# Performance work log

Measured on AMD Instinct MI355X. Metric: run time of the kernel, lower is better.

## Reference

```python
import jax, jax.numpy as jnp
import numpy as np

HIDDEN = 1024
HEADS = 16
HEAD_DIM = HIDDEN // HEADS


def rotate_half(x):
    x1, x2 = jnp.split(x, 2, axis=-1)
    return jnp.concatenate([-x2, x1], axis=-1)


def rope_cos_sin(T, head_dim):
    inv_freq = 1.0 / (10000.0 ** (jnp.arange(0, head_dim, 2, dtype=jnp.float32) / head_dim))
    pos = jnp.arange(T, dtype=jnp.float32)
    freqs = jnp.einsum('i,j->ij', pos, inv_freq)          # [T, head_dim/2]
    emb = jnp.concatenate([freqs, freqs], axis=-1)        # [T, head_dim]
    # broadcast shape [1, T, 1, head_dim]
    return jnp.cos(emb)[None, :, None, :], jnp.sin(emb)[None, :, None, :]


def setup_inputs() -> dict:
    key = jax.random.key(0)
    ks = jax.random.split(key, 9)
    B, T = 4, 2048
    s = 1.0 / np.sqrt(HIDDEN)
    x = jax.random.normal(ks[0], (B, T, HIDDEN), dtype=jnp.float32)
    Wq = jax.random.uniform(ks[1], (HIDDEN, HIDDEN), minval=-s, maxval=s, dtype=jnp.float32)
    bq = jax.random.uniform(ks[2], (HIDDEN,), minval=-s, maxval=s, dtype=jnp.float32)
    Wk = jax.random.uniform(ks[3], (HIDDEN, HIDDEN), minval=-s, maxval=s, dtype=jnp.float32)
    bk = jax.random.uniform(ks[4], (HIDDEN,), minval=-s, maxval=s, dtype=jnp.float32)
    Wv = jax.random.uniform(ks[5], (HIDDEN, HIDDEN), minval=-s, maxval=s, dtype=jnp.float32)
    bv = jax.random.uniform(ks[6], (HIDDEN,), minval=-s, maxval=s, dtype=jnp.float32)
    Wo = jax.random.uniform(ks[7], (HIDDEN, HIDDEN), minval=-s, maxval=s, dtype=jnp.float32)
    bo = jax.random.uniform(ks[8], (HIDDEN,), minval=-s, maxval=s, dtype=jnp.float32)
    return {"x": x, "Wq": Wq, "bq": bq, "Wk": Wk, "bk": bk,
            "Wv": Wv, "bv": bv, "Wo": Wo, "bo": bo}


def reference(x, Wq, bq, Wk, bk, Wv, bv, Wo, bo):
    B, T, _ = x.shape
    q = (x @ Wq + bq).reshape(B, T, HEADS, HEAD_DIM)
    k = (x @ Wk + bk).reshape(B, T, HEADS, HEAD_DIM)
    v = (x @ Wv + bv).reshape(B, T, HEADS, HEAD_DIM)
    cos, sin = rope_cos_sin(T, HEAD_DIM)
    q = q * cos + rotate_half(q) * sin
    k = k * cos + rotate_half(k) * sin
    scale = jnp.sqrt(jnp.float32(HEAD_DIM))
    scores = jnp.einsum('bqhd,bkhd->bhqk', q, k) / scale   # [B,H,T,T]
    causal = jnp.tril(jnp.ones((T, T), dtype=bool))
    scores = jnp.where(causal[None, None], scores, -jnp.inf)
    probs = jax.nn.softmax(scores, axis=-1)
    attn = jnp.einsum('bhqk,bkhd->bqhd', probs, v).reshape(B, T, HIDDEN)
    return attn @ Wo + bo
```

## Files before the change

### kernel.cpp

```cpp
#include <hip/hip_runtime.h>

typedef unsigned short u16;
typedef __attribute__((ext_vector_type(4))) float f32x4;
typedef __attribute__((ext_vector_type(16))) float f32x16;
typedef __attribute__((ext_vector_type(8))) short s16x8;

#define B_   4
#define T_   2048
#define H_   16
#define D_   64
#define HID  1024
#define BT   (B_*T_)
#define N3   3072

#define BARRIER() do { asm volatile("" ::: "memory"); __builtin_amdgcn_s_barrier(); asm volatile("" ::: "memory"); } while (0)

__device__ inline u16 f2b(float f) {
  union { float f; unsigned u; } v; v.f = f;
  unsigned u = v.u;
  unsigned r = (u + 0x7FFFu + ((u >> 16) & 1u)) >> 16;
  return (u16)r;
}

__device__ inline void gll16(const u16* g, u16* l) {
  __builtin_amdgcn_global_load_lds(
      (const __attribute__((address_space(1))) unsigned int*)g,
      (__attribute__((address_space(3))) unsigned int*)l, 16, 0, 0);
}

__device__ inline int swz8(int row) { return (row ^ (row >> 3)) & 7; }

__global__ void k_cast4(const float* __restrict__ src, u16* __restrict__ dst, int n4) {
  int i = blockIdx.x * blockDim.x + threadIdx.x;
  if (i >= n4) return;
  float4 v = ((const float4*)src)[i];
  ushort4 o;
  o.x = f2b(v.x); o.y = f2b(v.y); o.z = f2b(v.z); o.w = f2b(v.w);
  ((ushort4*)dst)[i] = o;
}

__global__ void k_ropetab(float2* __restrict__ tab) {
  int i = blockIdx.x * blockDim.x + threadIdx.x;
  int d = i & 31, t = i >> 5;
  float inv = expf(-0.28782313662425574f * (float)d);
  float ang = (float)t * inv;
  float c, s;
  sincosf(ang, &s, &c);
  tab[i] = make_float2(c, s);
}

__global__ __launch_bounds__(256) void k_packT(const float* __restrict__ W0,
                                               const float* __restrict__ W1,
                                               const float* __restrict__ W2,
                                               u16* __restrict__ Wt) {
  __shared__ float L[64][68];
  int n0 = blockIdx.x * 64, k0 = blockIdx.y * 64;
  int which = n0 >> 10;
  const float* W = (which == 0) ? W0 : (which == 1) ? W1 : W2;
  int nc = n0 & 1023;
  int tid = threadIdx.x;
  #pragma unroll
  for (int i = 0; i < 4; i++) {
    int ch = tid + 256 * i;
    int kr = ch >> 4, cc = ch & 15;
    float4 v = *(const float4*)(W + (size_t)(k0 + kr) * 1024 + nc + cc * 4);
    *(float4*)(&L[kr][cc * 4]) = v;
  }
  __syncthreads();
  #pragma unroll
  for (int i = 0; i < 2; i++) {
    int ch = tid + 256 * i;
    int nr = ch >> 3, ck = ch & 7;
    u16 tmp[8];
    #pragma unroll
    for (int j = 0; j < 8; j++) tmp[j] = f2b(L[ck * 8 + j][nr]);
    *(uint4*)(Wt + (size_t)(n0 + nr) * 1024 + k0 + ck * 8) = *(uint4*)tmp;
  }
}

__global__ __launch_bounds__(512, 2) void gemm256(
    const u16* __restrict__ A, const u16* __restrict__ Bt,
    const float* __restrict__ b0, const float* __restrict__ b1,
    const float* __restrict__ b2, const float2* __restrict__ tab,
    u16* __restrict__ outp)
{
  __shared__ __align__(16) char SM[135168];
  const int tid = threadIdx.x, lane = tid & 63, w = tid >> 6;
  const int l15 = lane & 15, g = lane >> 4;
  const int wm = (w >> 2) * 128, wn = (w & 3) * 64;
  const int mbase = blockIdx.y * 256, nbase = blockIdx.x * 256;
  const int K = 1024, NT = 16;
  f32x4 acc[8][4] = {};

  auto SHALF = [&](const u16* src, int base, int buf, int isB, int half, int t) {
    u16* dst = (u16*)(SM + buf * 65536 + isB * 32768 + half * 16384);
    #pragma unroll
    for (int i = 0; i < 2; i++) {
      int f = i * 512 + tid;
      int r = f >> 3, c = f & 7;
      int row = half * 128 + r;
      int cs = c ^ (row & 7);
      gll16(src + (size_t)(base + row) * K + t * 64 + cs * 8, dst + f * 8);
    }
  };
  auto RD = [&](const char* buf, int row, int kc) -> s16x8 {
    int slot = (kc * 4 + g) ^ (row & 7);
    return *(const s16x8*)(buf + row * 128 + slot * 16);
  };

  SHALF(A, mbase, 0, 0, 0, 0); SHALF(A, mbase, 0, 0, 1, 0);
  SHALF(Bt, nbase, 0, 1, 0, 0); SHALF(Bt, nbase, 0, 1, 1, 0);
  SHALF(Bt, nbase, 1, 1, 0, 1); SHALF(Bt, nbase, 1, 1, 1, 1);
  asm volatile("s_waitcnt vmcnt(4)" ::: "memory");
  BARRIER();

  s16x8 af[4][2], bf[4][2];
  for (int t = 0; t < NT; t++) {
    const char* Ab = SM + (t & 1) * 65536;
    const char* Bb = Ab + 32768;
    const int nxA = (t + 1) & 1;
    const int nxB = t & 1;

    #pragma unroll
    for (int mt = 0; mt < 4; mt++) {
      af[mt][0] = RD(Ab, wm + mt * 16 + l15, 0);
      af[mt][1] = RD(Ab, wm + mt * 16 + l15, 1);
    }
    #pragma unroll
    for (int nt = 0; nt < 2; nt++) {
      bf[nt][0] = RD(Bb, wn + nt * 16 + l15, 0);
      bf[nt][1] = RD(Bb, wn + nt * 16 + l15, 1);
    }
    if (t + 1 < NT) SHALF(A, mbase, nxA, 0, 0, t + 1);
    BARRIER();
    __builtin_amdgcn_s_setprio(1);
    #pragma unroll
    for (int mt = 0; mt < 4; mt++)
      #pragma unroll
      for (int nt = 0; nt < 2; nt++) {
        acc[mt][nt] = __builtin_amdgcn_mfma_f32_16x16x32_bf16(af[mt][0], bf[nt][0], acc[mt][nt], 0, 0, 0);
        acc[mt][nt] = __builtin_amdgcn_mfma_f32_16x16x32_bf16(af[mt][1], bf[nt][1], acc[mt][nt], 0, 0, 0);
      }
    __builtin_amdgcn_s_setprio(0);
    BARRIER();

    #pragma unroll
    for (int nt = 2; nt < 4; nt++) {
      bf[nt][0] = RD(Bb, wn + nt * 16 + l15, 0);
      bf[nt][1] = RD(Bb, wn + nt * 16 + l15, 1);
    }
    if (t + 1 < NT) SHALF(A, mbase, nxA, 0, 1, t + 1);
    BARRIER();
    __builtin_amdgcn_s_setprio(1);
    #pragma unroll
    for (int mt = 0; mt < 4; mt++)
      #pragma unroll
      for (int nt = 2; nt < 4; nt++) {
        acc[mt][nt] = __builtin_amdgcn_mfma_f32_16x16x32_bf16(af[mt][0], bf[nt][0], acc[mt][nt], 0, 0, 0);
        acc[mt][nt] = __builtin_amdgcn_mfma_f32_16x16x32_bf16(af[mt][1], bf[nt][1], acc[mt][nt], 0, 0, 0);
      }
    __builtin_amdgcn_s_setprio(0);
    BARRIER();

    #pragma unroll
    for (int mt = 0; mt < 4; mt++) {
      af[mt][0] = RD(Ab, wm + (mt + 4) * 16 + l15, 0);
      af[mt][1] = RD(Ab, wm + (mt + 4) * 16 + l15, 1);
    }
    if (t + 2 < NT) SHALF(Bt, nbase, nxB, 1, 0, t + 2);
    BARRIER();
    __builtin_amdgcn_s_setprio(1);
    #pragma unroll
    for (int mt = 0; mt < 4; mt++)
      #pragma unroll
      for (int nt = 0; nt < 2; nt++) {
        acc[mt + 4][nt] = __builtin_amdgcn_mfma_f32_16x16x32_bf16(af[mt][0], bf[nt][0], acc[mt + 4][nt], 0, 0, 0);
        acc[mt + 4][nt] = __builtin_amdgcn_mfma_f32_16x16x32_bf16(af[mt][1], bf[nt][1], acc[mt + 4][nt], 0, 0, 0);
      }
    __builtin_amdgcn_s_setprio(0);
    BARRIER();

    if (t + 2 < NT) SHALF(Bt, nbase, nxB, 1, 1, t + 2);
    BARRIER();
    __builtin_amdgcn_s_setprio(1);
    #pragma unroll
    for (int mt = 0; mt < 4; mt++)
      #pragma unroll
      for (int nt = 2; nt < 4; nt++) {
        acc[mt + 4][nt] = __builtin_amdgcn_mfma_f32_16x16x32_bf16(af[mt][0], bf[nt][0], acc[mt + 4][nt], 0, 0, 0);
        acc[mt + 4][nt] = __builtin_amdgcn_mfma_f32_16x16x32_bf16(af[mt][1], bf[nt][1], acc[mt + 4][nt], 0, 0, 0);
      }
    __builtin_amdgcn_s_setprio(0);
    if (t + 1 < NT) {
      if (t + 2 < NT) asm volatile("s_waitcnt vmcnt(4)" ::: "memory");
      else            asm volatile("s_waitcnt vmcnt(0)" ::: "memory");
    }
    BARRIER();
  }

  int which = nbase >> 10;
  const float* bp = (which == 0) ? b0 : (which == 1) ? b1 : b2;
  u16* Lt = (u16*)SM;
  BARRIER();
  if (which < 2) {
    const float FSC = (which == 0) ? 0.18033688011112043f : 1.0f;
    #pragma unroll
    for (int mt = 0; mt < 8; mt++) {
      #pragma unroll
      for (int r = 0; r < 4; r++) {
        int ml = wm + mt * 16 + g * 4 + r;
        int t = (mbase + ml) & (T_ - 1);
        #pragma unroll
        for (int nt = 0; nt < 2; nt++) {
          int d = nt * 16 + l15;
          float2 cs = tab[t * 32 + d];
          float a0 = acc[mt][nt][r]     + bp[(nbase + wn + d) & 1023];
          float a1 = acc[mt][nt + 2][r] + bp[(nbase + wn + d + 32) & 1023];
          Lt[ml * 264 + wn + d]      = f2b((a0 * cs.x - a1 * cs.y) * FSC);
          Lt[ml * 264 + wn + d + 32] = f2b((a1 * cs.x + a0 * cs.y) * FSC);
        }
      }
    }
    __syncthreads();
    #pragma unroll
    for (int i = 0; i < 16; i++) {
      int c = tid + 512 * i;
      int row = c >> 5, cc = c & 31;
      int gm = mbase + row, t = gm & (T_ - 1), bb = gm >> 11;
      int gn0 = nbase + cc * 8, h = (gn0 >> 6) & 15, d0 = gn0 & 63;
      *(uint4*)(outp + ((size_t)((which * B_ + bb) * H_ + h) * T_ + t) * D_ + d0) =
          *(const uint4*)(Lt + row * 264 + cc * 8);
    }
  } else {
    #pragma unroll
    for (int mt = 0; mt < 8; mt++) {
      #pragma unroll
      for (int nt = 0; nt < 4; nt++) {
        int nl = wn + nt * 16 + l15;
        float bias = bp[(nbase + nl) & 1023];
        u16 t4[4];
        #pragma unroll
        for (int r = 0; r < 4; r++) t4[r] = f2b(acc[mt][nt][r] + bias);
        *(uint2*)(Lt + nl * 264 + wm + mt * 16 + g * 4) = *(uint2*)t4;
      }
    }
    __syncthreads();
    #pragma unroll
    for (int i = 0; i < 16; i++) {
      int c = tid + 512 * i;
      int row = c >> 5, cc = c & 31;
      int gn = nbase + row, h = (gn >> 6) & 15, d = gn & 63;
      int m0 = mbase + cc * 8, bb = m0 >> 11, t0 = m0 & (T_ - 1);
      *(uint4*)(outp + ((size_t)((2 * B_ + bb) * H_ + h) * D_ + d) * T_ + t0) =
          *(const uint4*)(Lt + row * 264 + cc * 8);
    }
  }
}

template<int MODE>
__global__ __launch_bounds__(256) void gemm_k(
    const u16* __restrict__ A, const u16* __restrict__ Bt,
    const float* __restrict__ b0, void* __restrict__ outp, int N, int K)
{
  __shared__ __align__(16) u16 As[2][128 * 32];
  __shared__ __align__(16) u16 Bs[2][128 * 32];
  int tid = threadIdx.x, lane = tid & 63, w = tid >> 6;
  int l15 = lane & 15, g = lane >> 4;
  int wm = (w >> 1) * 64, wn = (w & 1) * 64;
  int mbase = blockIdx.y * 128, nbase = blockIdx.x * 128;
  f32x4 acc[4][4] = {};

  auto STAGE = [&](int bufi, int k0) {
    #pragma unroll
    for (int i = 0; i < 2; i++) {
      int f = i * 256 + tid;
      int row = f >> 2, c = f & 3;
      gll16(A  + (size_t)(mbase + row) * K + k0 + c * 8, &As[bufi][f * 8]);
      gll16(Bt + (size_t)(nbase + row) * K + k0 + c * 8, &Bs[bufi][f * 8]);
    }
  };

  STAGE(0, 0);
  int cur = 0;
  for (int k0 = 0; k0 < K; k0 += 32) {
    __syncthreads();
    if (k0 + 32 < K) STAGE(cur ^ 1, k0 + 32);
    s16x8 af[4], bf[4];
    #pragma unroll
    for (int mt = 0; mt < 4; mt++)
      af[mt] = *(const s16x8*)(&As[cur][(wm + mt * 16 + l15) * 32 + g * 8]);
    #pragma unroll
    for (int nt = 0; nt < 4; nt++)
      bf[nt] = *(const s16x8*)(&Bs[cur][(wn + nt * 16 + l15) * 32 + g * 8]);
    #pragma unroll
    for (int mt = 0; mt < 4; mt++)
      #pragma unroll
      for (int nt = 0; nt < 4; nt++)
        acc[mt][nt] = __builtin_amdgcn_mfma_f32_16x16x32_bf16(af[mt], bf[nt], acc[mt][nt], 0, 0, 0);
    cur ^= 1;
  }

  #pragma unroll
  for (int mt = 0; mt < 4; mt++)
    #pragma unroll
    for (int nt = 0; nt < 4; nt++)
      #pragma unroll
      for (int r = 0; r < 4; r++) {
        int gm = mbase + wm + mt * 16 + g * 4 + r;
        int gn = nbase + wn + nt * 16 + l15;
        ((float*)outp)[(size_t)gm * N + gn] = acc[mt][nt][r] + b0[gn];
      }
}

__global__ __launch_bounds__(512, 4) void k_flash(const u16* __restrict__ Qh,
                                                  const u16* __restrict__ Kh,
                                                  const u16* __restrict__ Vtg,
                                                  u16* __restrict__ O) {
  __shared__ __align__(16) char smem[65536];
  const int tid = threadIdx.x;
  const int lane = tid & 63;
  const int l31 = lane & 31, hi = lane >> 5;
  const int w = tid >> 6, grp = w >> 2, wi = w & 3;
  const int tidg = tid & 255;
  const int bh = blockIdx.x, p = blockIdx.y;
  const int b = bh >> 4, h = bh & 15;
  const size_t hb = (size_t)bh * T_ * D_;

  u16* kbase = (u16*)(smem + grp * 32768);

  const int f0 = tidg, f1 = 256 + tidg;
  const int r0 = f0 >> 3, c0 = (f0 & 7) ^ swz8(r0);
  const int r1 = f1 >> 3, c1 = (f1 & 7) ^ swz8(r1);
  const u16* kg0 = Kh + hb + (size_t)r0 * 64 + c0 * 8;
  const u16* kg1 = Kh + hb + (size_t)r1 * 64 + c1 * 8;
  const u16* vg0 = Vtg + hb + (size_t)r0 * T_ + c0 * 8;
  const u16* vg1 = Vtg + hb + (size_t)r1 * T_ + c1 * 8;

  auto STAGE = [&](int bufi, int kvblk) {
    u16* kb = kbase + bufi * 8192;
    int kv0 = kvblk * 64;
    gll16(kg0 + (size_t)kv0 * 64, kb + f0 * 8);
    gll16(kg1 + (size_t)kv0 * 64, kb + f1 * 8);
    gll16(vg0 + kv0, kb + 4096 + f0 * 8);
    gll16(vg1 + kv0, kb + 4096 + f1 * 8);
  };

  const int sw = (grp == 1) ? (2 * p + 2) : 17;
  int tile = (grp == 1) ? p : (15 - p);

  s16x8 qf[4];
  auto LOADQ = [&](int tl) {
    const u16* qp = Qh + hb + (size_t)(tl * 128 + wi * 32 + l31) * 64 + hi * 8;
    #pragma unroll
    for (int kc = 0; kc < 4; kc++) qf[kc] = *(const s16x8*)(qp + kc * 16);
  };
  LOADQ(tile);

  f32x16 o0 = {}, o1 = {};
  float l_ = 0.f;

  auto EPI = [&](int tl) {
    float inv = 1.0f / l_;
    int q = tl * 128 + wi * 32 + l31;
    size_t ob = ((size_t)b * T_ + q) * HID + h * 64 + hi * 4;
    #pragma unroll
    for (int k = 0; k < 4; k++) {
      u16 t4[4];
      #pragma unroll
      for (int j = 0; j < 4; j++) t4[j] = f2b(o0[k * 4 + j] * inv);
      *(uint2*)(O + ob + k * 8) = *(uint2*)t4;
      #pragma unroll
      for (int j = 0; j < 4; j++) t4[j] = f2b(o1[k * 4 + j] * inv);
      *(uint2*)(O + ob + 32 + k * 8) = *(uint2*)t4;
    }
  };

  STAGE(0, 0);
  for (int i = 0; i < 17; i++) {
    __syncthreads();
    if (i + 1 < 17) {
      int nb = (i + 1 < sw) ? (i + 1) : (17 + (i + 1) - sw);
      STAGE((i + 1) & 1, nb);
    }
    if (grp == 1 && i == sw) {
      EPI(tile);
      f32x16 z = {};
      o0 = z; o1 = z; l_ = 0.f;
      tile = 15 - p;
      LOADQ(tile);
    }
    int kvblk = (i < sw) ? i : (17 + i - sw);
    int kv0 = kvblk * 64;
    int qw0 = tile * 128 + wi * 32;
    if (kv0 > qw0 + 31) continue;

    const char* Kb = (const char*)kbase + (i & 1) * 16384;
    const char* Vb = Kb + 8192;

    f32x16 S0 = {}, S1 = {};
    const int swzl = swz8(l31) << 4, swzh = swz8(32 + l31) << 4;
    __builtin_amdgcn_s_setprio(1);
    #pragma unroll
    for (int kc = 0; kc < 4; kc++) {
      s16x8 kf0 = *(const s16x8*)(Kb + ((l31 * 128 + kc * 32 + hi * 16) ^ swzl));
      s16x8 kf1 = *(const s16x8*)(Kb + (((32 + l31) * 128 + kc * 32 + hi * 16) ^ swzh));
      S0 = __builtin_amdgcn_mfma_f32_32x32x16_bf16(kf0, qf[kc], S0, 0, 0, 0);
      S1 = __builtin_amdgcn_mfma_f32_32x32x16_bf16(kf1, qf[kc], S1, 0, 0, 0);
    }
    __builtin_amdgcn_s_setprio(0);

    if (kv0 + 63 > qw0) {
      int qrel = qw0 + l31 - kv0 - 4 * hi;
      #pragma unroll
      for (int r = 0; r < 16; r++) {
        const int kvr = (r & 3) + 8 * (r >> 2);
        if (kvr > qrel)      S0[r] = -__builtin_inff();
        if (kvr + 32 > qrel) S1[r] = -__builtin_inff();
      }
    }

    float rs = 0.f;
    __builtin_amdgcn_s_setprio(1);
    #pragma unroll
    for (int h2 = 0; h2 < 2; h2++) {
      #pragma unroll
      for (int cc = 0; cc < 2; cc++) {
        float e[8];
        #pragma unroll
        for (int j = 0; j < 8; j++) {
          int r = cc * 8 + j;
          e[j] = __builtin_exp2f(h2 ? S1[r] : S0[r]);
          rs += e[j];
        }
        unsigned p0, p1, p2, p3;
        asm("v_cvt_pk_bf16_f32 %0, %1, %2" : "=v"(p0) : "v"(e[0]), "v"(e[1]));
        asm("v_cvt_pk_bf16_f32 %0, %1, %2" : "=v"(p1) : "v"(e[2]), "v"(e[3]));
        asm("v_cvt_pk_bf16_f32 %0, %1, %2" : "=v"(p2) : "v"(e[4]), "v"(e[5]));
        asm("v_cvt_pk_bf16_f32 %0, %1, %2" : "=v"(p3) : "v"(e[6]), "v"(e[7]));
        asm("v_permlane32_swap_b32 %0, %1" : "+v"(p0), "+v"(p2));
        asm("v_permlane32_swap_b32 %0, %1" : "+v"(p1), "+v"(p3));
        union { unsigned u[4]; s16x8 v; } pb;
        pb.u[0] = p0; pb.u[1] = p1; pb.u[2] = p2; pb.u[3] = p3;
        const int kk = h2 * 2 + cc;
        s16x8 vf0 = *(const s16x8*)(Vb + ((l31 * 128 + kk * 32 + hi * 16) ^ swzl));
        s16x8 vf1 = *(const s16x8*)(Vb + (((32 + l31) * 128 + kk * 32 + hi * 16) ^ swzh));
        o0 = __builtin_amdgcn_mfma_f32_32x32x16_bf16(vf0, pb.v, o0, 0, 0, 0);
        o1 = __builtin_amdgcn_mfma_f32_32x32x16_bf16(vf1, pb.v, o1, 0, 0, 0);
      }
    }
    __builtin_amdgcn_s_setprio(0);
    rs += __shfl_xor(rs, 32);
    l_ += rs;
  }

  __syncthreads();
  float* mb = (float*)smem;
  if (grp == 1) {
    float* rrow = mb + (wi * 64 + lane) * 36;
    #pragma unroll
    for (int k = 0; k < 4; k++) {
      f32x4 v0, v1;
      #pragma unroll
      for (int j = 0; j < 4; j++) { v0[j] = o0[k * 4 + j]; v1[j] = o1[k * 4 + j]; }
      *(f32x4*)(rrow + k * 4) = v0;
      *(f32x4*)(rrow + 16 + k * 4) = v1;
    }
    rrow[32] = l_;
  }
  __syncthreads();
  if (grp == 0) {
    float* rrow = mb + (wi * 64 + lane) * 36;
    l_ += rrow[32];
    #pragma unroll
    for (int k = 0; k < 4; k++) {
      f32x4 v0 = *(const f32x4*)(rrow + k * 4);
      f32x4 v1 = *(const f32x4*)(rrow + 16 + k * 4);
      #pragma unroll
      for (int j = 0; j < 4; j++) {
        o0[k * 4 + j] += v0[j];
        o1[k * 4 + j] += v1[j];
      }
    }
    EPI(15 - p);
  }
}

extern "C" void kernel_launch(void* const* d_in, const int* in_sizes, int n_in,
                              void* d_out, int out_size, void* d_ws, size_t ws_size,
                              hipStream_t stream) {
  const float* x  = (const float*)d_in[0];
  const float* Wq = (const float*)d_in[1];
  const float* bq = (const float*)d_in[2];
  const float* Wk = (const float*)d_in[3];
  const float* bk = (const float*)d_in[4];
  const float* Wv = (const float*)d_in[5];
  const float* bv = (const float*)d_in[6];
  const float* Wo = (const float*)d_in[7];
  const float* bo = (const float*)d_in[8];
  float* out = (float*)d_out;

  char* ws = (char*)d_ws;
  u16* xb    = (u16*)(ws);
  u16* WqkvT = (u16*)(ws + (size_t)16777216);
  u16* WoT   = (u16*)(ws + (size_t)16777216 + 6291456);
  u16* QKVh  = (u16*)(ws + (size_t)16777216 + 6291456 + 2097152);
  u16* Oattn = xb;
  float2* tab = (float2*)WoT;

  k_cast4<<<(BT * HID / 4 + 255) / 256, 256, 0, stream>>>(x, xb, BT * HID / 4);
  k_packT<<<dim3(N3 / 64, HID / 64), 256, 0, stream>>>(Wq, Wk, Wv, WqkvT);
  k_ropetab<<<256, 256, 0, stream>>>(tab);

  gemm256<<<dim3(N3 / 256, BT / 256), 512, 0, stream>>>(
      xb, WqkvT, bq, bk, bv, tab, QKVh);

  k_packT<<<dim3(HID / 64, HID / 64), 256, 0, stream>>>(Wo, Wo, Wo, WoT);

  k_flash<<<dim3(B_ * H_, 8), 512, 0, stream>>>(
      QKVh, QKVh + (size_t)BT * HID, QKVh + 2 * (size_t)BT * HID, Oattn);

  gemm_k<1><<<dim3(HID / 128, BT / 128), 256, 0, stream>>>(
      Oattn, WoT, bo, (void*)out, HID, HID);
}
```

Baseline: 185.9 us.

## Swizzle GEMM block order, compute softmax row sums via MFMA, preload second Q tile

Both GEMM kernels remap linear block IDs so that consecutively scheduled blocks share input tiles, aiming for better L2 reuse. In the attention kernel, the per-row softmax denominator is now accumulated by an extra MFMA against a ones vector, using the same bf16-rounded probabilities as the PV product. This replaces the scalar adds and the cross-lane shuffle. The second Q tile is also loaded into registers up front instead of being reloaded mid-loop. The extra MFMA per chunk and the added 16-float accumulator raise register pressure and matrix-core work.

```diff
diff --git a/kernel.cpp b/kernel.cpp
--- a/kernel.cpp
+++ b/kernel.cpp
@@ -88,7 +88,9 @@
   const int tid = threadIdx.x, lane = tid & 63, w = tid >> 6;
   const int l15 = lane & 15, g = lane >> 4;
   const int wm = (w >> 2) * 128, wn = (w & 3) * 64;
-  const int mbase = blockIdx.y * 256, nbase = blockIdx.x * 256;
+  const int orig = blockIdx.y * 12 + blockIdx.x;
+  const int swzb = (orig & 7) * 48 + (orig >> 3);
+  const int mbase = (swzb / 12) * 256, nbase = (swzb % 12) * 256;
   const int K = 1024, NT = 16;
   f32x4 acc[8][4] = {};
 
@@ -267,7 +269,9 @@
   int tid = threadIdx.x, lane = tid & 63, w = tid >> 6;
   int l15 = lane & 15, g = lane >> 4;
   int wm = (w >> 1) * 64, wn = (w & 1) * 64;
-  int mbase = blockIdx.y * 128, nbase = blockIdx.x * 128;
+  int orig = blockIdx.y * 8 + blockIdx.x;
+  int swzb = (orig & 7) * 64 + (orig >> 3);
+  int mbase = (swzb >> 3) * 128, nbase = (swzb & 7) * 128;
   f32x4 acc[4][4] = {};
 
   auto STAGE = [&](int bufi, int k0) {
@@ -348,19 +352,24 @@
   const int sw = (grp == 1) ? (2 * p + 2) : 17;
   int tile = (grp == 1) ? p : (15 - p);
 
-  s16x8 qf[4];
-  auto LOADQ = [&](int tl) {
-    const u16* qp = Qh + hb + (size_t)(tl * 128 + wi * 32 + l31) * 64 + hi * 8;
+  s16x8 qf[4], qfB[4];
+  {
+    const u16* qp = Qh + hb + (size_t)(tile * 128 + wi * 32 + l31) * 64 + hi * 8;
     #pragma unroll
     for (int kc = 0; kc < 4; kc++) qf[kc] = *(const s16x8*)(qp + kc * 16);
-  };
-  LOADQ(tile);
-
-  f32x16 o0 = {}, o1 = {};
-  float l_ = 0.f;
-
-  auto EPI = [&](int tl) {
-    float inv = 1.0f / l_;
+    const u16* qp2 = Qh + hb + (size_t)((15 - p) * 128 + wi * 32 + l31) * 64 + hi * 8;
+    #pragma unroll
+    for (int kc = 0; kc < 4; kc++) qfB[kc] = *(const s16x8*)(qp2 + kc * 16);
+  }
+
+  s16x8 onesv;
+  #pragma unroll
+  for (int i = 0; i < 8; i++) onesv[i] = (short)0x3F80;
+
+  f32x16 o0 = {}, o1 = {}, lacc = {};
+
+  auto EPI = [&](int tl, float lsum) {
+    float inv = 1.0f / lsum;
     int q = tl * 128 + wi * 32 + l31;
     size_t ob = ((size_t)b * T_ + q) * HID + h * 64 + hi * 4;
     #pragma unroll
@@ -383,11 +392,12 @@
       STAGE((i + 1) & 1, nb);
     }
     if (grp == 1 && i == sw) {
-      EPI(tile);
+      EPI(tile, lacc[0]);
       f32x16 z = {};
-      o0 = z; o1 = z; l_ = 0.f;
+      o0 = z; o1 = z; lacc = z;
       tile = 15 - p;
-      LOADQ(tile);
+      #pragma unroll
+      for (int kc = 0; kc < 4; kc++) qf[kc] = qfB[kc];
     }
     int kvblk = (i < sw) ? i : (17 + i - sw);
     int kv0 = kvblk * 64;
@@ -419,7 +429,6 @@
       }
     }
 
-    float rs = 0.f;
     __builtin_amdgcn_s_setprio(1);
     #pragma unroll
     for (int h2 = 0; h2 < 2; h2++) {
@@ -430,7 +439,6 @@
         for (int j = 0; j < 8; j++) {
           int r = cc * 8 + j;
           e[j] = __builtin_exp2f(h2 ? S1[r] : S0[r]);
-          rs += e[j];
         }
         unsigned p0, p1, p2, p3;
         asm("v_cvt_pk_bf16_f32 %0, %1, %2" : "=v"(p0) : "v"(e[0]), "v"(e[1]));
@@ -446,11 +454,10 @@
         s16x8 vf1 = *(const s16x8*)(Vb + (((32 + l31) * 128 + kk * 32 + hi * 16) ^ swzh));
         o0 = __builtin_amdgcn_mfma_f32_32x32x16_bf16(vf0, pb.v, o0, 0, 0, 0);
         o1 = __builtin_amdgcn_mfma_f32_32x32x16_bf16(vf1, pb.v, o1, 0, 0, 0);
+        lacc = __builtin_amdgcn_mfma_f32_32x32x16_bf16(onesv, pb.v, lacc, 0, 0, 0);
       }
     }
     __builtin_amdgcn_s_setprio(0);
-    rs += __shfl_xor(rs, 32);
-    l_ += rs;
   }
 
   __syncthreads();
@@ -465,12 +472,12 @@
       *(f32x4*)(rrow + k * 4) = v0;
       *(f32x4*)(rrow + 16 + k * 4) = v1;
     }
-    rrow[32] = l_;
+    rrow[32] = lacc[0];
   }
   __syncthreads();
   if (grp == 0) {
     float* rrow = mb + (wi * 64 + lane) * 36;
-    l_ += rrow[32];
+    float lsum = lacc[0] + rrow[32];
     #pragma unroll
     for (int k = 0; k < 4; k++) {
       f32x4 v0 = *(const f32x4*)(rrow + k * 4);
@@ -481,7 +488,7 @@
         o1[k * 4 + j] += v1[j];
       }
     }
-    EPI(15 - p);
+    EPI(15 - p, lsum);
   }
 }
 
```

Measured after the change: 208.1 us. 11.9% more time.
